# Optimization experiments

Measured on AMD Instinct MI355X. Metric: run time of the kernel, lower is better.

The kernel has to match this reference:

```python
import jax, jax.numpy as jnp
import numpy as np

N = 50000      # nodes
E = 400000     # edges (avg degree 8)
N_IN = 256     # n_in_chan
N_HID = 256    # n_hid_chan


def gcn_conv(x, src, dst, W, b, n):
    """PyG GCNConv: D^{-1/2}(A+I)D^{-1/2} X W^T + b (add_self_loops=True, unit weights)."""
    h = x @ W.T                                           # [n, out]
    # degree over A + I: each node has a self loop (the initial ones) plus in-edges
    deg = jnp.ones((n,), h.dtype).at[dst].add(1.0)        # [n]
    dinv = jax.lax.rsqrt(deg)                             # deg >= 1 always
    norm = dinv[src] * dinv[dst]                          # [E]
    agg = jnp.zeros_like(h).at[dst].add(h[src] * norm[:, None])
    agg = agg + h * (dinv * dinv)[:, None]                # self-loop term, norm = dinv_i^2
    return agg + b


def setup_inputs() -> dict:
    key = jax.random.key(0)
    k1, k2, k3, k4 = jax.random.split(key, 4)
    x = jax.random.normal(k1, (N, N_IN + N_HID), dtype=jnp.float32)
    edge_index = jax.random.randint(k2, (2, E), 0, N, dtype=jnp.int64)
    s1 = 1.0 / np.sqrt(N_IN + N_HID)
    s2 = 1.0 / np.sqrt(N_HID)
    W1 = jax.random.normal(k3, (N_HID, N_IN + N_HID), dtype=jnp.float32) * s1
    W2 = jax.random.normal(k4, (N_HID, N_HID), dtype=jnp.float32) * s2
    b1 = jnp.zeros((N_HID,), jnp.float32)
    b2 = jnp.zeros((N_HID,), jnp.float32)
    return {"x": x, "edge_index": edge_index, "W1": W1, "b1": b1, "W2": W2, "b2": b2}


def reference(x, edge_index, W1, b1, W2, b2):
    src, dst = edge_index[0], edge_index[1]
    h = jax.nn.relu(gcn_conv(x, src, dst, W1, b1, N))
    return gcn_conv(h, src, dst, W2, b2, N)
```

## Files before the change

kernel.cpp:

```cpp
#include <hip/hip_runtime.h>
#include <hip/hip_bf16.h>

#define NN 50000
#define CH 256
#define SLOTS 96
#define G1K 512
#define G2K 256

typedef unsigned short u16;
typedef unsigned int   u32;

using short8 = __attribute__((ext_vector_type(8))) short;
using u16x8  = __attribute__((ext_vector_type(8))) unsigned short;
using f32x4  = __attribute__((ext_vector_type(4))) float;

static __device__ __forceinline__ float4 ld4(const float* p){ return *(const float4*)p; }

static __device__ __forceinline__ u16 f2b(float f){
  u32 u = __float_as_uint(f);
  u = (u + 0x7fffu + ((u >> 16) & 1u)) >> 16;
  return (u16)u;
}
static __device__ __forceinline__ float b2f(u16 b){
  return __uint_as_float(((u32)b) << 16);
}
static __device__ __forceinline__ int pkbf(float lo, float hi){
  __hip_bfloat162 h = __float22bfloat162_rn(make_float2(lo, hi));
  int r; __builtin_memcpy(&r, &h, 4); return r;
}

static __device__ __forceinline__ void gload_lds16(const void* g, void* l){
  __builtin_amdgcn_global_load_lds((const __attribute__((address_space(1))) void*)g,
                                   (__attribute__((address_space(3))) void*)l, 16, 0, 0);
}

#define WBAR(vm) do{ \
    asm volatile("s_waitcnt vmcnt(" #vm ") lgkmcnt(0)" ::: "memory"); \
    __builtin_amdgcn_s_barrier(); \
  }while(0)


__global__ void ell_build_kernel(const int* __restrict__ src, const int* __restrict__ dst,
                                 int* __restrict__ deg, int* __restrict__ ell, int E,
                                 const float* __restrict__ W1, u16* __restrict__ W1bf, int w1n4,
                                 const float* __restrict__ W2, u16* __restrict__ W2bf, int w2n4){
  int T = gridDim.x * 256;
  int g = blockIdx.x*256 + threadIdx.x;
  if (g < E){
    int d = dst[g];
    int pos = atomicAdd(&deg[d], 1);
    if (pos < SLOTS) ell[(size_t)d*SLOTS + pos] = src[g];
  }
  for (int i = g; i < w1n4; i += T){
    float4 v = ld4(W1 + (size_t)i*4);
    int2 o = { pkbf(v.x,v.y), pkbf(v.z,v.w) };
    *(int2*)(W1bf + (size_t)i*4) = o;
  }
  for (int i = g; i < w2n4; i += T){
    float4 v = ld4(W2 + (size_t)i*4);
    int2 o = { pkbf(v.x,v.y), pkbf(v.z,v.w) };
    *(int2*)(W2bf + (size_t)i*4) = o;
  }
}


#define G1_GLB_B(kt, bb) do{ \
    gload_lds16(gB + (size_t)(kt)*32,          &Bs[bb][wave*2048]); \
    gload_lds16(gB + (size_t)(kt)*32 + 16*G1K, &Bs[bb][wave*2048 + 512]); \
    gload_lds16(gB + (size_t)(kt)*32 + 32*G1K, &Bs[bb][wave*2048 + 1024]); \
    gload_lds16(gB + (size_t)(kt)*32 + 48*G1K, &Bs[bb][wave*2048 + 1536]); \
  }while(0)

#define G1_GLB_A(kt, ab) do{ \
    gload_lds16(gA0 + (size_t)(kt)*32, &Asf[ab][wave*512]); \
    gload_lds16(gA1 + (size_t)(kt)*32, &Asf[ab][wave*512 + 256]); \
  }while(0)

#define G1_COMP(ra, rb) do{ \
    short8 af[4], bq[4]; \
    _Pragma("unroll") \
    for (int i=0;i<4;i++){ \
      int r = i*16 + lm; \
      float4 f0 = *(const float4*)&Asf[ra][r*32 + ((s0 ^ (lm&7))<<2)]; \
      float4 f1 = *(const float4*)&Asf[ra][r*32 + ((s1 ^ (lm&7))<<2)]; \
      int4 p = { pkbf(f0.x,f0.y), pkbf(f0.z,f0.w), pkbf(f1.x,f1.y), pkbf(f1.z,f1.w) }; \
      af[i] = *(short8*)&p; \
    } \
    _Pragma("unroll") \
    for (int j=0;j<4;j++) bq[j] = *(const short8*)&Bs[rb][(wave*64 + j*16 + lm)*32 + lk]; \
    _Pragma("unroll") \
    for (int i=0;i<4;i++) \
      _Pragma("unroll") \
      for (int j=0;j<4;j++) \
        acc[i][j] = __builtin_amdgcn_mfma_f32_16x16x32_bf16(af[i], bq[j], acc[i][j], 0, 0, 0); \
  }while(0)

__global__ __launch_bounds__(256, 2) void gemm1_kernel(const float* __restrict__ A,
                                                       const u16* __restrict__ Bbf,
                                                       const int* __restrict__ deg,
                                                       u16* __restrict__ C, int M){
  __shared__ float Asf[3][64*32];
  __shared__ u16   Bs[2][256*32];
  int tid = threadIdx.x;
  int wave = tid >> 6, lane = tid & 63;
  int bm = blockIdx.x;

  int cslot = (lane & 7) ^ (lane >> 3);
  int r0 = bm*64 + wave*16 + (lane>>3);     if (r0 > M-1) r0 = M-1;
  int r1 = r0 + 8;                          if (r1 > M-1) r1 = M-1;
  const float* gA0 = A + (size_t)r0*G1K + cslot*4;
  const float* gA1 = A + (size_t)r1*G1K + cslot*4;
  const u16* gB = Bbf + (size_t)(wave*64 + (lane>>2))*G1K + (lane&3)*8;

  int lm = lane & 15;
  int lk = (lane >> 4) * 8;
  int s0 = (lane >> 4) * 2;
  int s1 = s0 + 1;

  f32x4 acc[4][4] = {};

  G1_GLB_B(0, 0);
  G1_GLB_A(0, 0);
  G1_GLB_A(1, 1);
  WBAR(2);

  G1_GLB_B( 1,1); G1_COMP(0,0); G1_GLB_A( 2,2); WBAR(2);
  G1_GLB_B( 2,0); G1_COMP(1,1); G1_GLB_A( 3,0); WBAR(2);
  G1_GLB_B( 3,1); G1_COMP(2,0); G1_GLB_A( 4,1); WBAR(2);
  G1_GLB_B( 4,0); G1_COMP(0,1); G1_GLB_A( 5,2); WBAR(2);
  G1_GLB_B( 5,1); G1_COMP(1,0); G1_GLB_A( 6,0); WBAR(2);
  G1_GLB_B( 6,0); G1_COMP(2,1); G1_GLB_A( 7,1); WBAR(2);
  G1_GLB_B( 7,1); G1_COMP(0,0); G1_GLB_A( 8,2); WBAR(2);
  G1_GLB_B( 8,0); G1_COMP(1,1); G1_GLB_A( 9,0); WBAR(2);
  G1_GLB_B( 9,1); G1_COMP(2,0); G1_GLB_A(10,1); WBAR(2);
  G1_GLB_B(10,0); G1_COMP(0,1); G1_GLB_A(11,2); WBAR(2);
  G1_GLB_B(11,1); G1_COMP(1,0); G1_GLB_A(12,0); WBAR(2);
  G1_GLB_B(12,0); G1_COMP(2,1); G1_GLB_A(13,1); WBAR(2);
  G1_GLB_B(13,1); G1_COMP(0,0); G1_GLB_A(14,2); WBAR(2);
  G1_GLB_B(14,0); G1_COMP(1,1); G1_GLB_A(15,0); WBAR(2);
  G1_GLB_B(15,1); G1_COMP(2,0);                 WBAR(0);
                  G1_COMP(0,1);

  int rb = (lane >> 4) * 4;
  #pragma unroll
  for (int i=0;i<4;i++){
    #pragma unroll
    for (int r=0;r<4;r++){
      int row = bm*64 + i*16 + rb + r;
      if (row < M){
        float dr = rsqrtf(1.0f + (float)deg[row]);
        #pragma unroll
        for (int j=0;j<4;j++){
          int col = wave*64 + j*16 + lm;
          C[(size_t)row*CH + col] = f2b(acc[i][j][r] * dr);
        }
      }
    }
  }
}


#define G2_GLB(kt, bb) do{ \
    gload_lds16(gA + (size_t)(kt)*32,          &As2[bb][wave*512]); \
    gload_lds16(gB + (size_t)(kt)*32,          &Bs2[bb][wave*2048]); \
    gload_lds16(gB + (size_t)(kt)*32 + 16*G2K, &Bs2[bb][wave*2048 + 512]); \
    gload_lds16(gB + (size_t)(kt)*32 + 32*G2K, &Bs2[bb][wave*2048 + 1024]); \
    gload_lds16(gB + (size_t)(kt)*32 + 48*G2K, &Bs2[bb][wave*2048 + 1536]); \
  }while(0)

#define G2_COMP(rb) do{ \
    short8 af[4], bq[4]; \
    _Pragma("unroll") \
    for (int i=0;i<4;i++) af[i] = *(const short8*)&As2[rb][(i*16 + lm)*32 + lk]; \
    _Pragma("unroll") \
    for (int j=0;j<4;j++) bq[j] = *(const short8*)&Bs2[rb][(wave*64 + j*16 + lm)*32 + lk]; \
    _Pragma("unroll") \
    for (int i=0;i<4;i++) \
      _Pragma("unroll") \
      for (int j=0;j<4;j++) \
        acc[i][j] = __builtin_amdgcn_mfma_f32_16x16x32_bf16(af[i], bq[j], acc[i][j], 0, 0, 0); \
  }while(0)

__global__ __launch_bounds__(256, 4) void gemm2_kernel(const u16* __restrict__ A,
                                                       const u16* __restrict__ B,
                                                       float* __restrict__ Cout,
                                                       const float* __restrict__ bias, int M){
  __shared__ u16 As2[3][64*32];
  __shared__ u16 Bs2[3][256*32];
  int tid = threadIdx.x;
  int wave = tid >> 6, lane = tid & 63;
  int bm = blockIdx.x;

  int ar = bm*64 + wave*16 + (lane>>2); if (ar > M-1) ar = M-1;
  const u16* gA = A + (size_t)ar*G2K + (lane&3)*8;
  const u16* gB = B + (size_t)(wave*64 + (lane>>2))*G2K + (lane&3)*8;

  int lm = lane & 15;
  int lk = (lane >> 4) * 8;

  f32x4 acc[4][4] = {};

  G2_GLB(0, 0);
  G2_GLB(1, 1);
  WBAR(5);

  G2_GLB(2,2); G2_COMP(0); WBAR(5);
  G2_GLB(3,0); G2_COMP(1); WBAR(5);
  G2_GLB(4,1); G2_COMP(2); WBAR(5);
  G2_GLB(5,2); G2_COMP(0); WBAR(5);
  G2_GLB(6,0); G2_COMP(1); WBAR(5);
  G2_GLB(7,1); G2_COMP(2); WBAR(5);
               G2_COMP(0); WBAR(0);
               G2_COMP(1);

  float bv[4];
  #pragma unroll
  for (int j=0;j<4;j++) bv[j] = bias[wave*64 + j*16 + lm];

  int rb = (lane >> 4) * 4;
  #pragma unroll
  for (int i=0;i<4;i++){
    #pragma unroll
    for (int r=0;r<4;r++){
      int row = bm*64 + i*16 + rb + r;
      if (row < M){
        #pragma unroll
        for (int j=0;j<4;j++){
          int col = wave*64 + j*16 + lm;
          Cout[(size_t)row*CH + col] = acc[i][j][r] + bv[j];
        }
      }
    }
  }
}


template<bool RELU, bool BIAS, bool SCALEOUT>
__global__ __launch_bounds__(256) void aggregate_kernel(const u16* __restrict__ h,
                                                        const float* __restrict__ bias,
                                                        const int* __restrict__ deg,
                                                        const int* __restrict__ ell,
                                                        u16* __restrict__ outv, int n){
  int wave = threadIdx.x >> 6;
  int lane = threadIdx.x & 63;
  int i = blockIdx.x*4 + wave;
  if (i >= n) return;
  int half = lane >> 5;
  int c = (lane & 31) * 8;

  int degi = deg[i];
  float di = rsqrtf(1.0f + (float)degi);
  int m = degi < SLOTS ? degi : SLOTS;
  const int* row = ell + (size_t)i*SLOTS;

  float acc[8];
  #pragma unroll
  for (int k=0;k<8;k++) acc[k] = 0.f;

  int e = half;
  for (; e + 6 < m; e += 8){
    int s0 = row[e], s1 = row[e+2], s2 = row[e+4], s3 = row[e+6];
    u16x8 h0 = *(const u16x8*)(h + (size_t)s0*CH + c);
    u16x8 h1 = *(const u16x8*)(h + (size_t)s1*CH + c);
    u16x8 h2 = *(const u16x8*)(h + (size_t)s2*CH + c);
    u16x8 h3 = *(const u16x8*)(h + (size_t)s3*CH + c);
    #pragma unroll
    for (int k=0;k<8;k++) acc[k] += b2f(h0[k]);
    #pragma unroll
    for (int k=0;k<8;k++) acc[k] += b2f(h1[k]);
    #pragma unroll
    for (int k=0;k<8;k++) acc[k] += b2f(h2[k]);
    #pragma unroll
    for (int k=0;k<8;k++) acc[k] += b2f(h3[k]);
  }
  for (; e < m; e += 2){
    int s0 = row[e];
    u16x8 h0 = *(const u16x8*)(h + (size_t)s0*CH + c);
    #pragma unroll
    for (int k=0;k<8;k++) acc[k] += b2f(h0[k]);
  }

  if (half == 0){
    u16x8 hv = *(const u16x8*)(h + (size_t)i*CH + c);
    #pragma unroll
    for (int k=0;k<8;k++) acc[k] += b2f(hv[k]);
  }

  #pragma unroll
  for (int k=0;k<8;k++) acc[k] += __shfl_xor(acc[k], 32, 64);

  if (half == 0){
    float bv[8];
    if (BIAS){
      float4 b0 = ld4(bias + c), b1 = ld4(bias + c + 4);
      bv[0]=b0.x; bv[1]=b0.y; bv[2]=b0.z; bv[3]=b0.w;
      bv[4]=b1.x; bv[5]=b1.y; bv[6]=b1.z; bv[7]=b1.w;
    }
    u16x8 o;
    #pragma unroll
    for (int k=0;k<8;k++){
      float v = acc[k] * di;
      if (BIAS) v += bv[k];
      if (RELU) v = fmaxf(v, 0.f);
      if (SCALEOUT) v *= di;
      o[k] = f2b(v);
    }
    *(u16x8*)(outv + (size_t)i*CH + c) = o;
  }
}


extern "C" void kernel_launch(void* const* d_in, const int* in_sizes, int n_in,
                              void* d_out, int out_size, void* d_ws, size_t ws_size,
                              hipStream_t stream){
  const float* x  = (const float*)d_in[0];
  const int*   ei = (const int*)d_in[1];
  const float* W1 = (const float*)d_in[2];
  const float* b1 = (const float*)d_in[3];
  const float* W2 = (const float*)d_in[4];
  const float* b2 = (const float*)d_in[5];
  float* out = (float*)d_out;

  const int n = NN;
  const int E = in_sizes[1] / 2;
  const int* src = ei;
  const int* dst = ei + E;

  char* ws = (char*)d_ws;
  size_t off = 0;
  auto alloc = [&](size_t bytes)->char* {
    char* p = ws + off;
    off += (bytes + 255) & ~(size_t)255;
    return p;
  };
  u16*   h1bf   = (u16*)  alloc((size_t)n*CH*sizeof(u16));
  u16*   h2bf   = (u16*)  alloc((size_t)n*CH*sizeof(u16));
  u16*   W1bf   = (u16*)  alloc((size_t)CH*G1K*sizeof(u16));
  u16*   W2bf   = (u16*)  alloc((size_t)CH*CH*sizeof(u16));
  int*   deg    = (int*)  alloc((size_t)n*sizeof(int));
  int*   ell    = (int*)  alloc((size_t)n*SLOTS*sizeof(int));
  (void)ws_size;

  u16* g1out = (u16*)d_out;

  hipMemsetAsync(deg, 0, (size_t)n*sizeof(int), stream);
  ell_build_kernel<<<(E+255)/256, 256, 0, stream>>>(src, dst, deg, ell, E,
                                                    W1, W1bf, CH*G1K/4,
                                                    W2, W2bf, CH*CH/4);

  dim3 gg((n+63)/64);

  gemm1_kernel<<<gg, 256, 0, stream>>>(x, W1bf, deg, g1out, n);
  aggregate_kernel<true, true, true><<<(n+3)/4, 256, 0, stream>>>(g1out, b1, deg, ell, h1bf, n);

  aggregate_kernel<false, false, false><<<(n+3)/4, 256, 0, stream>>>(h1bf, b2, deg, ell, h2bf, n);
  gemm2_kernel<<<gg, 256, 0, stream>>>(h2bf, W2bf, out, b2, n);
}
```

Measured before the change: 319.9 us.

## Deepen GEMM1 prefetch pipeline, add sched barriers, simplify aggregate lane mapping

GEMM1 grows from two to three B buffers and from three to four A buffers, so loads are issued two k-steps ahead (waitcnt 8) to hide more global latency. Scheduling barriers after the global-to-LDS load groups in both GEMMs keep the compiler from interleaving them with compute. The aggregate kernel now has each lane own 4 channels across the whole row, with a scalarized node index and no half-wave split or cross-half shuffle, trading 16-byte gathers for 8-byte gathers. The larger LDS footprint may lower GEMM1 occupancy.

```diff
diff --git a/kernel.cpp b/kernel.cpp
--- a/kernel.cpp
+++ b/kernel.cpp
@@ -38,6 +38,8 @@
     asm volatile("s_waitcnt vmcnt(" #vm ") lgkmcnt(0)" ::: "memory"); \
     __builtin_amdgcn_s_barrier(); \
   }while(0)
+
+#define SCHED0 __builtin_amdgcn_sched_barrier(0)
 
 
 __global__ void ell_build_kernel(const int* __restrict__ src, const int* __restrict__ dst,
@@ -69,11 +71,13 @@
     gload_lds16(gB + (size_t)(kt)*32 + 16*G1K, &Bs[bb][wave*2048 + 512]); \
     gload_lds16(gB + (size_t)(kt)*32 + 32*G1K, &Bs[bb][wave*2048 + 1024]); \
     gload_lds16(gB + (size_t)(kt)*32 + 48*G1K, &Bs[bb][wave*2048 + 1536]); \
+    SCHED0; \
   }while(0)
 
 #define G1_GLB_A(kt, ab) do{ \
     gload_lds16(gA0 + (size_t)(kt)*32, &Asf[ab][wave*512]); \
     gload_lds16(gA1 + (size_t)(kt)*32, &Asf[ab][wave*512 + 256]); \
+    SCHED0; \
   }while(0)
 
 #define G1_COMP(ra, rb) do{ \
@@ -99,8 +103,8 @@
                                                        const u16* __restrict__ Bbf,
                                                        const int* __restrict__ deg,
                                                        u16* __restrict__ C, int M){
-  __shared__ float Asf[3][64*32];
-  __shared__ u16   Bs[2][256*32];
+  __shared__ float Asf[4][64*32];
+  __shared__ u16   Bs[3][256*32];
   int tid = threadIdx.x;
   int wave = tid >> 6, lane = tid & 63;
   int bm = blockIdx.x;
@@ -121,25 +125,27 @@
 
   G1_GLB_B(0, 0);
   G1_GLB_A(0, 0);
+  G1_GLB_B(1, 1);
   G1_GLB_A(1, 1);
-  WBAR(2);
-
-  G1_GLB_B( 1,1); G1_COMP(0,0); G1_GLB_A( 2,2); WBAR(2);
-  G1_GLB_B( 2,0); G1_COMP(1,1); G1_GLB_A( 3,0); WBAR(2);
-  G1_GLB_B( 3,1); G1_COMP(2,0); G1_GLB_A( 4,1); WBAR(2);
-  G1_GLB_B( 4,0); G1_COMP(0,1); G1_GLB_A( 5,2); WBAR(2);
-  G1_GLB_B( 5,1); G1_COMP(1,0); G1_GLB_A( 6,0); WBAR(2);
-  G1_GLB_B( 6,0); G1_COMP(2,1); G1_GLB_A( 7,1); WBAR(2);
-  G1_GLB_B( 7,1); G1_COMP(0,0); G1_GLB_A( 8,2); WBAR(2);
-  G1_GLB_B( 8,0); G1_COMP(1,1); G1_GLB_A( 9,0); WBAR(2);
-  G1_GLB_B( 9,1); G1_COMP(2,0); G1_GLB_A(10,1); WBAR(2);
-  G1_GLB_B(10,0); G1_COMP(0,1); G1_GLB_A(11,2); WBAR(2);
-  G1_GLB_B(11,1); G1_COMP(1,0); G1_GLB_A(12,0); WBAR(2);
-  G1_GLB_B(12,0); G1_COMP(2,1); G1_GLB_A(13,1); WBAR(2);
-  G1_GLB_B(13,1); G1_COMP(0,0); G1_GLB_A(14,2); WBAR(2);
-  G1_GLB_B(14,0); G1_COMP(1,1); G1_GLB_A(15,0); WBAR(2);
-  G1_GLB_B(15,1); G1_COMP(2,0);                 WBAR(0);
-                  G1_COMP(0,1);
+  G1_GLB_A(2, 2);
+  WBAR(8);
+
+  G1_GLB_B( 2,2); G1_COMP(0,0); G1_GLB_A( 3,3); WBAR(8);
+  G1_GLB_B( 3,0); G1_COMP(1,1); G1_GLB_A( 4,0); WBAR(8);
+  G1_GLB_B( 4,1); G1_COMP(2,2); G1_GLB_A( 5,1); WBAR(8);
+  G1_GLB_B( 5,2); G1_COMP(3,0); G1_GLB_A( 6,2); WBAR(8);
+  G1_GLB_B( 6,0); G1_COMP(0,1); G1_GLB_A( 7,3); WBAR(8);
+  G1_GLB_B( 7,1); G1_COMP(1,2); G1_GLB_A( 8,0); WBAR(8);
+  G1_GLB_B( 8,2); G1_COMP(2,0); G1_GLB_A( 9,1); WBAR(8);
+  G1_GLB_B( 9,0); G1_COMP(3,1); G1_GLB_A(10,2); WBAR(8);
+  G1_GLB_B(10,1); G1_COMP(0,2); G1_GLB_A(11,3); WBAR(8);
+  G1_GLB_B(11,2); G1_COMP(1,0); G1_GLB_A(12,0); WBAR(8);
+  G1_GLB_B(12,0); G1_COMP(2,1); G1_GLB_A(13,1); WBAR(8);
+  G1_GLB_B(13,1); G1_COMP(3,2); G1_GLB_A(14,2); WBAR(8);
+  G1_GLB_B(14,2); G1_COMP(0,0); G1_GLB_A(15,3); WBAR(8);
+  G1_GLB_B(15,0); G1_COMP(1,1);                 WBAR(6);
+                  G1_COMP(2,2);                 WBAR(0);
+                  G1_COMP(3,0);
 
   int rb = (lane >> 4) * 4;
   #pragma unroll
@@ -166,6 +172,7 @@
     gload_lds16(gB + (size_t)(kt)*32 + 16*G2K, &Bs2[bb][wave*2048 + 512]); \
     gload_lds16(gB + (size_t)(kt)*32 + 32*G2K, &Bs2[bb][wave*2048 + 1024]); \
     gload_lds16(gB + (size_t)(kt)*32 + 48*G2K, &Bs2[bb][wave*2048 + 1536]); \
+    SCHED0; \
   }while(0)
 
 #define G2_COMP(rb) do{ \
@@ -245,68 +252,50 @@
   int lane = threadIdx.x & 63;
   int i = blockIdx.x*4 + wave;
   if (i >= n) return;
-  int half = lane >> 5;
-  int c = (lane & 31) * 8;
+  i = __builtin_amdgcn_readfirstlane(i);
 
   int degi = deg[i];
   float di = rsqrtf(1.0f + (float)degi);
   int m = degi < SLOTS ? degi : SLOTS;
-  const int* row = ell + (size_t)i*SLOTS;
-
-  float acc[8];
-  #pragma unroll
-  for (int k=0;k<8;k++) acc[k] = 0.f;
-
-  int e = half;
-  for (; e + 6 < m; e += 8){
-    int s0 = row[e], s1 = row[e+2], s2 = row[e+4], s3 = row[e+6];
-    u16x8 h0 = *(const u16x8*)(h + (size_t)s0*CH + c);
-    u16x8 h1 = *(const u16x8*)(h + (size_t)s1*CH + c);
-    u16x8 h2 = *(const u16x8*)(h + (size_t)s2*CH + c);
-    u16x8 h3 = *(const u16x8*)(h + (size_t)s3*CH + c);
-    #pragma unroll
-    for (int k=0;k<8;k++) acc[k] += b2f(h0[k]);
-    #pragma unroll
-    for (int k=0;k<8;k++) acc[k] += b2f(h1[k]);
-    #pragma unroll
-    for (int k=0;k<8;k++) acc[k] += b2f(h2[k]);
-    #pragma unroll
-    for (int k=0;k<8;k++) acc[k] += b2f(h3[k]);
-  }
-  for (; e < m; e += 2){
-    int s0 = row[e];
-    u16x8 h0 = *(const u16x8*)(h + (size_t)s0*CH + c);
-    #pragma unroll
-    for (int k=0;k<8;k++) acc[k] += b2f(h0[k]);
-  }
-
-  if (half == 0){
-    u16x8 hv = *(const u16x8*)(h + (size_t)i*CH + c);
-    #pragma unroll
-    for (int k=0;k<8;k++) acc[k] += b2f(hv[k]);
-  }
-
-  #pragma unroll
-  for (int k=0;k<8;k++) acc[k] += __shfl_xor(acc[k], 32, 64);
-
-  if (half == 0){
-    float bv[8];
-    if (BIAS){
-      float4 b0 = ld4(bias + c), b1 = ld4(bias + c + 4);
-      bv[0]=b0.x; bv[1]=b0.y; bv[2]=b0.z; bv[3]=b0.w;
-      bv[4]=b1.x; bv[5]=b1.y; bv[6]=b1.z; bv[7]=b1.w;
-    }
-    u16x8 o;
-    #pragma unroll
-    for (int k=0;k<8;k++){
-      float v = acc[k] * di;
-      if (BIAS) v += bv[k];
-      if (RELU) v = fmaxf(v, 0.f);
-      if (SCALEOUT) v *= di;
-      o[k] = f2b(v);
-    }
-    *(u16x8*)(outv + (size_t)i*CH + c) = o;
-  }
+  const int* __restrict__ row = ell + (size_t)i*SLOTS;
+  int c = lane * 4;
+
+  float a0=0.f, a1=0.f, a2=0.f, a3=0.f;
+
+  int e = 0;
+  for (; e + 3 < m; e += 4){
+    int j0 = row[e], j1 = row[e+1], j2 = row[e+2], j3 = row[e+3];
+    ushort4 h0 = *(const ushort4*)(h + (size_t)j0*CH + c);
+    ushort4 h1 = *(const ushort4*)(h + (size_t)j1*CH + c);
+    ushort4 h2 = *(const ushort4*)(h + (size_t)j2*CH + c);
+    ushort4 h3 = *(const ushort4*)(h + (size_t)j3*CH + c);
+    a0 += b2f(h0.x) + b2f(h1.x) + b2f(h2.x) + b2f(h3.x);
+    a1 += b2f(h0.y) + b2f(h1.y) + b2f(h2.y) + b2f(h3.y);
+    a2 += b2f(h0.z) + b2f(h1.z) + b2f(h2.z) + b2f(h3.z);
+    a3 += b2f(h0.w) + b2f(h1.w) + b2f(h2.w) + b2f(h3.w);
+  }
+  for (; e < m; ++e){
+    int j0 = row[e];
+    ushort4 h0 = *(const ushort4*)(h + (size_t)j0*CH + c);
+    a0 += b2f(h0.x); a1 += b2f(h0.y); a2 += b2f(h0.z); a3 += b2f(h0.w);
+  }
+
+  ushort4 hv = *(const ushort4*)(h + (size_t)i*CH + c);
+  a0 += b2f(hv.x); a1 += b2f(hv.y); a2 += b2f(hv.z); a3 += b2f(hv.w);
+
+  float v0 = a0*di, v1 = a1*di, v2 = a2*di, v3 = a3*di;
+  if (BIAS){
+    float4 b = ld4(bias + c);
+    v0 += b.x; v1 += b.y; v2 += b.z; v3 += b.w;
+  }
+  if (RELU){
+    v0 = fmaxf(v0, 0.f); v1 = fmaxf(v1, 0.f);
+    v2 = fmaxf(v2, 0.f); v3 = fmaxf(v3, 0.f);
+  }
+  if (SCALEOUT){ v0 *= di; v1 *= di; v2 *= di; v3 *= di; }
+
+  ushort4 o; o.x = f2b(v0); o.y = f2b(v1); o.z = f2b(v2); o.w = f2b(v3);
+  *(ushort4*)(outv + (size_t)i*CH + c) = o;
 }
 
 
```

After: 306.7 us. 1.04x faster.
